# Performance work log

Hardware: AMD Instinct MI355X
Metric: run time of the kernel (lower is better)

The kernel has to match this reference:

```python
import jax, jax.numpy as jnp
import numpy as np

NEURON_CDECAY = 0.5
NEURON_VDECAY = 0.75
NEURON_VTH = 0.5
SPIKE_PSEUDO_GRAD_WINDOW = 0.5

@jax.custom_vjp
def pseudo_spike(v):
    return (v > NEURON_VTH).astype(v.dtype)

def _ps_fwd(v):
    return pseudo_spike(v), v

def _ps_bwd(v, g):
    return (g * (jnp.abs(v - NEURON_VTH) < SPIKE_PSEUDO_GRAD_WINDOW).astype(g.dtype),)

pseudo_spike.defvjp(_ps_fwd, _ps_bwd)

def conv1d(x, w, b):
    # x: (B, Cin, L), w: (Cout, Cin, K), stride 2, VALID padding
    y = jax.lax.conv_general_dilated(x, w, window_strides=(2,), padding='VALID',
                                     dimension_numbers=('NCH', 'OIH', 'NCH'))
    return y + b[None, :, None]

def neuron(syn_out, u, v, s):
    u = u * NEURON_CDECAY + syn_out
    v = v * NEURON_VDECAY * (1.0 - s) + u
    s = pseudo_spike(v)
    return u, v, s

def setup_inputs() -> dict:
    key = jax.random.key(0)
    ks = jax.random.split(key, 18)
    B, T, L = 4096, 50, 360
    h1, h2, h3, A = 256, 256, 128, 2
    def w(k, shape, fan_in):
        bound = 1.0 / np.sqrt(fan_in)
        return jax.random.uniform(k, shape, jnp.float32, -bound, bound)
    return {
        'normal_spikes': (jax.random.uniform(ks[0], (B, 6, T)) < 0.5).astype(jnp.float32),
        'scan_spikes': (jax.random.uniform(ks[1], (B, 1, L, T)) < 0.5).astype(jnp.float32),
        'batch_size': B,
        'conv1_w': w(ks[2], (5, 1, 5), 5),   'conv1_b': w(ks[3], (5,), 5),
        'conv2_w': w(ks[4], (5, 5, 5), 25),  'conv2_b': w(ks[5], (5,), 25),
        'conv3_w': w(ks[6], (5, 5, 5), 25),  'conv3_b': w(ks[7], (5,), 25),
        'fc1_w': w(ks[8], (h1, 216), 216),   'fc1_b': w(ks[9], (h1,), 216),
        'fc2_w': w(ks[10], (h2, h1), h1),    'fc2_b': w(ks[11], (h2,), h1),
        'fc3_w': w(ks[12], (h3, h2), h2),    'fc3_b': w(ks[13], (h3,), h2),
        'fc4_w': w(ks[14], (A, h3), h3),     'fc4_b': w(ks[15], (A,), h3),
    }

def reference(normal_spikes, scan_spikes, batch_size,
              conv1_w, conv1_b, conv2_w, conv2_b, conv3_w, conv3_b,
              fc1_w, fc1_b, fc2_w, fc2_b, fc3_w, fc3_b, fc4_w, fc4_b):
    B = batch_size
    T = normal_spikes.shape[-1]
    A = fc4_w.shape[0]
    # time-major sequences for lax.scan
    scan_seq = jnp.moveaxis(scan_spikes, -1, 0)    # (T, B, 1, 360)
    norm_seq = jnp.moveaxis(normal_spikes, -1, 0)  # (T, B, 6)

    z = lambda *s: jnp.zeros(s, jnp.float32)
    init = (
        (z(B, 5, 178), z(B, 5, 178), z(B, 5, 178)),
        (z(B, 5, 87),  z(B, 5, 87),  z(B, 5, 87)),
        (z(B, 5, 42),  z(B, 5, 42),  z(B, 5, 42)),
        (z(B, 256), z(B, 256), z(B, 256)),
        (z(B, 256), z(B, 256), z(B, 256)),
        (z(B, 128), z(B, 128), z(B, 128)),
        (z(B, A),   z(B, A),   z(B, A)),
        z(B, A),
    )

    def step(carry, xs):
        c1, c2, c3, f1, f2, f3, f4, acc = carry
        scan_x, norm_x = xs
        c1 = neuron(conv1d(scan_x, conv1_w, conv1_b), *c1)
        c2 = neuron(conv1d(c1[2], conv2_w, conv2_b), *c2)
        c3 = neuron(conv1d(c2[2], conv3_w, conv3_b), *c3)
        comb = jnp.concatenate([c3[2].reshape(B, -1), norm_x], axis=1)  # (B, 216)
        f1 = neuron(comb @ fc1_w.T + fc1_b, *f1)
        f2 = neuron(f1[2] @ fc2_w.T + fc2_b, *f2)
        f3 = neuron(f2[2] @ fc3_w.T + fc3_b, *f3)
        f4 = neuron(f3[2] @ fc4_w.T + fc4_b, *f4)
        acc = acc + f4[2]
        return (c1, c2, c3, f1, f2, f3, f4, acc), None

    carry, _ = jax.lax.scan(step, init, (scan_seq, norm_seq))
    return carry[-1] / T
```

## Files before the change

kernel.cpp:

```cpp
#include <hip/hip_runtime.h>
#include <cstdint>
#include <cstddef>


#define NB 4096
#define MTOT (NB * 50)

__device__ __forceinline__ void neuron_update(float syn, float& u, float& v, float& s) {
    u = u * 0.5f + syn;
    v = v * 0.75f * (1.0f - s) + u;
    s = (v > 0.5f) ? 1.0f : 0.0f;
}

__global__ __launch_bounds__(192) void conv1_kernel(
    const float* __restrict__ x, const float* __restrict__ w1,
    const float* __restrict__ b1, unsigned long long* __restrict__ S1)
{
    __shared__ float xl[9000];
    const int tid = threadIdx.x;
    const int b = blockIdx.x;
    const int j = tid;
    const int lbase = (j < 178) ? 2 * j : 354;

    float wr[25], br[5];
#pragma unroll
    for (int q = 0; q < 25; ++q) wr[q] = w1[q];
#pragma unroll
    for (int o = 0; o < 5; ++o) br[o] = b1[o];

    float u[5], v[5], s[5];
#pragma unroll
    for (int o = 0; o < 5; ++o) { u[o] = 0.f; v[o] = 0.f; s[o] = 0.f; }

    const float* xb = x + (size_t)b * 18000;
    for (int half = 0; half < 2; ++half) {
        const int t0 = half * 25;
        __syncthreads();
        for (int e = tid; e < 9000; e += 192)
            xl[e] = xb[(e / 25) * 50 + t0 + (e % 25)];
        __syncthreads();
        for (int dt = 0; dt < 25; ++dt) {
            const int t = t0 + dt;
            float xv[5];
#pragma unroll
            for (int k = 0; k < 5; ++k) xv[k] = xl[(lbase + k) * 25 + dt];
#pragma unroll
            for (int o = 0; o < 5; ++o) {
                float syn = 0.f;
#pragma unroll
                for (int k = 0; k < 5; ++k) syn += wr[o * 5 + k] * xv[k];
                syn += br[o];
                neuron_update(syn, u[o], v[o], s[o]);
                unsigned long long m = __ballot(j < 178 && s[o] > 0.5f);
                if ((tid & 63) == 0)
                    S1[(((size_t)b * 50 + t) * 5 + o) * 3 + (tid >> 6)] = m;
            }
        }
    }
}

__global__ __launch_bounds__(128) void conv2_kernel(
    const unsigned int* __restrict__ S1, const float* __restrict__ w2,
    const float* __restrict__ b2, unsigned int* __restrict__ S2)
{
    __shared__ unsigned int s1l[1501];
    const int tid = threadIdx.x;
    const int b = blockIdx.x;

    float wr[125], br[5];
#pragma unroll
    for (int q = 0; q < 125; ++q) wr[q] = w2[q];
#pragma unroll
    for (int o = 0; o < 5; ++o) br[o] = b2[o];

    const unsigned int* src = S1 + (size_t)b * 1500;
    for (int e = tid; e < 1500; e += 128) s1l[e] = src[e];
    __syncthreads();

    const int p = (tid < 87) ? 2 * tid : 172;
    const int pw = p >> 5, ps = p & 31;

    float u[5], v[5], s[5];
#pragma unroll
    for (int o = 0; o < 5; ++o) { u[o] = 0.f; v[o] = 0.f; s[o] = 0.f; }

    for (int t = 0; t < 50; ++t) {
        float xv[25];
#pragma unroll
        for (int ci = 0; ci < 5; ++ci) {
            const int base = (t * 5 + ci) * 6 + pw;
            unsigned long long bits =
                ((((unsigned long long)s1l[base + 1]) << 32) | (unsigned long long)s1l[base]) >> ps;
#pragma unroll
            for (int k = 0; k < 5; ++k)
                xv[ci * 5 + k] = ((bits >> k) & 1ULL) ? 1.0f : 0.0f;
        }
#pragma unroll
        for (int o = 0; o < 5; ++o) {
            float syn = 0.f;
#pragma unroll
            for (int q = 0; q < 25; ++q) syn += wr[o * 25 + q] * xv[q];
            syn += br[o];
            neuron_update(syn, u[o], v[o], s[o]);
            unsigned long long m = __ballot(tid < 87 && s[o] > 0.5f);
            const size_t outb = (((size_t)b * 50 + t) * 5 + o) * 3;
            if (tid == 0) {
                S2[outb]     = (unsigned int)m;
                S2[outb + 1] = (unsigned int)(m >> 32);
            }
            if (tid == 64) S2[outb + 2] = (unsigned int)m;
        }
    }
}

__global__ __launch_bounds__(64) void conv3_kernel(
    const unsigned int* __restrict__ S2, const float* __restrict__ w3,
    const float* __restrict__ b3, const float* __restrict__ normal,
    unsigned int* __restrict__ ST0)
{
    __shared__ unsigned int s2l[751];
    const int tid = threadIdx.x;
    const int b = blockIdx.x;

    float wr[125], br[5];
#pragma unroll
    for (int q = 0; q < 125; ++q) wr[q] = w3[q];
#pragma unroll
    for (int o = 0; o < 5; ++o) br[o] = b3[o];

    const unsigned int* src = S2 + (size_t)b * 750;
    for (int e = tid; e < 750; e += 64) s2l[e] = src[e];
    __syncthreads();

    const int p = (tid < 42) ? 2 * tid : 82;
    const int pw = p >> 5, ps = p & 31;

    float u[5], v[5], s[5];
#pragma unroll
    for (int o = 0; o < 5; ++o) { u[o] = 0.f; v[o] = 0.f; s[o] = 0.f; }

    for (int t = 0; t < 50; ++t) {
        float xv[25];
#pragma unroll
        for (int ci = 0; ci < 5; ++ci) {
            const int base = (t * 5 + ci) * 3 + pw;
            unsigned long long bits =
                ((((unsigned long long)s2l[base + 1]) << 32) | (unsigned long long)s2l[base]) >> ps;
#pragma unroll
            for (int k = 0; k < 5; ++k)
                xv[ci * 5 + k] = ((bits >> k) & 1ULL) ? 1.0f : 0.0f;
        }
        unsigned long long m[5];
#pragma unroll
        for (int o = 0; o < 5; ++o) {
            float syn = 0.f;
#pragma unroll
            for (int q = 0; q < 25; ++q) syn += wr[o * 25 + q] * xv[q];
            syn += br[o];
            neuron_update(syn, u[o], v[o], s[o]);
            m[o] = __ballot(tid < 42 && s[o] > 0.5f);
        }
        const unsigned long long nm =
            __ballot(tid < 6 && normal[((size_t)b * 6 + tid) * 50 + t] > 0.5f);
        if (tid == 0) {
            const unsigned long long r0 = m[0] | (m[1] << 42);
            const unsigned long long r1 = (m[1] >> 22) | (m[2] << 20) | (m[3] << 62);
            const unsigned long long r2 = (m[3] >> 2) | (m[4] << 40);
            const unsigned long long r3 = (m[4] >> 24) | (nm << 18);
            const size_t mrow = (size_t)b * 50 + t;
            ST0[0 * (size_t)MTOT + mrow] = (unsigned int)r0;
            ST0[1 * (size_t)MTOT + mrow] = (unsigned int)(r0 >> 32);
            ST0[2 * (size_t)MTOT + mrow] = (unsigned int)r1;
            ST0[3 * (size_t)MTOT + mrow] = (unsigned int)(r1 >> 32);
            ST0[4 * (size_t)MTOT + mrow] = (unsigned int)r2;
            ST0[5 * (size_t)MTOT + mrow] = (unsigned int)(r2 >> 32);
            ST0[6 * (size_t)MTOT + mrow] = (unsigned int)r3;
        }
    }
}

__global__ __launch_bounds__(256) void transpose_w_kernel(
    const float* __restrict__ W, float* __restrict__ Wt, int N, int KREAL, int KPAD)
{
    const int idx = blockIdx.x * 256 + threadIdx.x;
    if (idx >= KPAD * N) return;
    const int k = idx / N, n = idx % N;
    Wt[idx] = (k < KREAL) ? W[(size_t)n * KREAL + k] : 0.f;
}

__global__ __launch_bounds__(256) void sgemm_bits_kernel(
    const uint32_t* __restrict__ bitsT,
    const float* __restrict__ Wt,
    const float* __restrict__ bias,
    float* __restrict__ syn,
    int Ntot, int KT, int row0)
{
    const int tid = threadIdx.x;
    const int mloc = blockIdx.x * 256 + tid;
    const int mg = row0 + mloc;
    const int nbase = blockIdx.y * 32;

    uint32_t aw[8];
#pragma unroll
    for (int w = 0; w < 8; ++w)
        aw[w] = (w < KT) ? bitsT[(size_t)w * MTOT + mg] : 0u;

    float acc[32];
#pragma unroll
    for (int j = 0; j < 32; ++j) acc[j] = 0.f;

    const float* wt = Wt + nbase;
    for (int kt = 0; kt < KT; ++kt) {
        const uint32_t abit = aw[kt];
        const float* wk = wt + (size_t)(kt * 32) * Ntot;
#pragma unroll
        for (int kk = 0; kk < 32; ++kk) {
            const float a = (float)((abit >> kk) & 1u);
            const float* wr = wk + (size_t)kk * Ntot;
#pragma unroll
            for (int j = 0; j < 32; ++j)
                acc[j] = fmaf(a, wr[j], acc[j]);
        }
    }

    float* so = syn + (size_t)mloc * Ntot + nbase;
    const float* bs = bias + nbase;
#pragma unroll
    for (int q = 0; q < 8; ++q) {
        float4 ov;
        ov.x = acc[q * 4 + 0] + bs[q * 4 + 0];
        ov.y = acc[q * 4 + 1] + bs[q * 4 + 1];
        ov.z = acc[q * 4 + 2] + bs[q * 4 + 2];
        ov.w = acc[q * 4 + 3] + bs[q * 4 + 3];
        *reinterpret_cast<float4*>(so + q * 4) = ov;
    }
}

__global__ __launch_bounds__(256) void fc_scanT_kernel(
    const float* __restrict__ syn,
    uint32_t* __restrict__ SFT,
    int b0)
{
    const int tid = threadIdx.x;
    const int lane = tid & 63;
    const int ob = tid >> 6;
    const int bl = blockIdx.x;
    const int o = ob * 64 + lane;

    float u = 0.f, v = 0.f, s = 0.f;
    for (int t = 0; t < 50; ++t) {
        const float sv = syn[((size_t)bl * 50 + t) * 256 + o];
        neuron_update(sv, u, v, s);
        const unsigned long long m = __ballot(s > 0.5f);
        if (lane == 0) {
            const size_t row = (size_t)(b0 + bl) * 50 + t;
            SFT[(size_t)(2 * ob) * MTOT + row]     = (uint32_t)m;
            SFT[(size_t)(2 * ob + 1) * MTOT + row] = (uint32_t)(m >> 32);
        }
    }
}

__global__ __launch_bounds__(256) void fc_scan128_kernel(
    const float* __restrict__ syn,
    unsigned long long* __restrict__ SF,
    int b0)
{
    const int tid = threadIdx.x;
    const int wid = blockIdx.x * 4 + (tid >> 6);
    const int lane = tid & 63;
    const int bl = wid >> 1;
    const int ob = wid & 1;
    const int o = ob * 64 + lane;

    float u = 0.f, v = 0.f, s = 0.f;
    for (int t = 0; t < 50; ++t) {
        const float sv = syn[((size_t)bl * 50 + t) * 128 + o];
        neuron_update(sv, u, v, s);
        const unsigned long long m = __ballot(s > 0.5f);
        if (lane == 0) SF[((size_t)(b0 + bl) * 50 + t) * 2 + ob] = m;
    }
}

__global__ __launch_bounds__(256) void fc4_gemm_kernel(
    const unsigned long long* __restrict__ SF3, const float* __restrict__ W,
    const float* __restrict__ bias, float* __restrict__ syn4)
{
    const int m = blockIdx.x * 256 + threadIdx.x;
    const unsigned long long w0 = SF3[(size_t)m * 2];
    const unsigned long long w1 = SF3[(size_t)m * 2 + 1];
    float a0 = 0.f, a1 = 0.f;
#pragma unroll
    for (int i = 0; i < 64; ++i) {
        const float bit = ((w0 >> i) & 1ULL) ? 1.f : 0.f;
        a0 = fmaf(bit, W[i], a0);
        a1 = fmaf(bit, W[128 + i], a1);
    }
#pragma unroll
    for (int i = 0; i < 64; ++i) {
        const float bit = ((w1 >> i) & 1ULL) ? 1.f : 0.f;
        a0 = fmaf(bit, W[64 + i], a0);
        a1 = fmaf(bit, W[192 + i], a1);
    }
    syn4[(size_t)m * 2]     = a0 + bias[0];
    syn4[(size_t)m * 2 + 1] = a1 + bias[1];
}

__global__ __launch_bounds__(64) void fc4_scan_kernel(
    const float* __restrict__ syn4, float* __restrict__ out)
{
    const int b = blockIdx.x * 64 + threadIdx.x;
    float u0 = 0.f, v0 = 0.f, s0 = 0.f, acc0 = 0.f;
    float u1 = 0.f, v1 = 0.f, s1 = 0.f, acc1 = 0.f;
    for (int t = 0; t < 50; ++t) {
        const float x0 = syn4[((size_t)b * 50 + t) * 2];
        const float x1 = syn4[((size_t)b * 50 + t) * 2 + 1];
        neuron_update(x0, u0, v0, s0); acc0 += s0;
        neuron_update(x1, u1, v1, s1); acc1 += s1;
    }
    out[b * 2]     = acc0 / 50.0f;
    out[b * 2 + 1] = acc1 / 50.0f;
}

extern "C" void kernel_launch(void* const* d_in, const int* in_sizes, int n_in,
                              void* d_out, int out_size, void* d_ws, size_t ws_size,
                              hipStream_t stream) {
    (void)in_sizes; (void)n_in; (void)out_size;
    const float* normal = (const float*)d_in[0];
    const float* xscan  = (const float*)d_in[1];
    const float* w1  = (const float*)d_in[3];
    const float* b1  = (const float*)d_in[4];
    const float* w2  = (const float*)d_in[5];
    const float* b2  = (const float*)d_in[6];
    const float* w3  = (const float*)d_in[7];
    const float* b3  = (const float*)d_in[8];
    const float* fw1 = (const float*)d_in[9];
    const float* fb1 = (const float*)d_in[10];
    const float* fw2 = (const float*)d_in[11];
    const float* fb2 = (const float*)d_in[12];
    const float* fw3 = (const float*)d_in[13];
    const float* fb3 = (const float*)d_in[14];
    const float* fw4 = (const float*)d_in[15];
    const float* fb4 = (const float*)d_in[16];
    float* out = (float*)d_out;

    char* wp = (char*)d_ws;
    size_t off = 0;
    auto take = [&](size_t bytes) -> void* {
        void* p = wp + off;
        off += (bytes + 255) & ~(size_t)255;
        return p;
    };
    float* Wt1 = (float*)take((size_t)224 * 256 * 4);
    float* Wt2 = (float*)take((size_t)256 * 256 * 4);
    float* Wt3 = (float*)take((size_t)256 * 128 * 4);
    unsigned long long* S1  = (unsigned long long*)take((size_t)NB * 50 * 15 * 8);
    unsigned int*       S2  = (unsigned int*)take((size_t)NB * 50 * 15 * 4);
    uint32_t* ST0 = (uint32_t*)take((size_t)8 * MTOT * 4);
    uint32_t* ST1 = (uint32_t*)take((size_t)8 * MTOT * 4);
    uint32_t* ST2 = (uint32_t*)take((size_t)8 * MTOT * 4);
    unsigned long long* SF3 = (unsigned long long*)take((size_t)MTOT * 2 * 8);
    float*              syn4 = (float*)take((size_t)MTOT * 2 * 4);

    int chunk = NB;
    while (chunk > 128 && off + (size_t)chunk * 50 * 256 * 4 > ws_size) chunk >>= 1;
    float* syn = (float*)take((size_t)chunk * 50 * 256 * 4);

    transpose_w_kernel<<<(224 * 256 + 255) / 256, 256, 0, stream>>>(fw1, Wt1, 256, 216, 224);
    transpose_w_kernel<<<(256 * 256 + 255) / 256, 256, 0, stream>>>(fw2, Wt2, 256, 256, 256);
    transpose_w_kernel<<<(256 * 128 + 255) / 256, 256, 0, stream>>>(fw3, Wt3, 128, 256, 256);

    conv1_kernel<<<NB, 192, 0, stream>>>(xscan, w1, b1, S1);
    conv2_kernel<<<NB, 128, 0, stream>>>((const unsigned int*)S1, w2, b2, S2);
    conv3_kernel<<<NB, 64, 0, stream>>>(S2, w3, b3, normal, ST0);

    for (int b0 = 0; b0 < NB; b0 += chunk) {
        sgemm_bits_kernel<<<dim3(chunk * 50 / 256, 8), 256, 0, stream>>>(
            ST0, Wt1, fb1, syn, 256, 7, b0 * 50);
        fc_scanT_kernel<<<chunk, 256, 0, stream>>>(syn, ST1, b0);
    }
    for (int b0 = 0; b0 < NB; b0 += chunk) {
        sgemm_bits_kernel<<<dim3(chunk * 50 / 256, 8), 256, 0, stream>>>(
            ST1, Wt2, fb2, syn, 256, 8, b0 * 50);
        fc_scanT_kernel<<<chunk, 256, 0, stream>>>(syn, ST2, b0);
    }
    for (int b0 = 0; b0 < NB; b0 += chunk) {
        sgemm_bits_kernel<<<dim3(chunk * 50 / 256, 4), 256, 0, stream>>>(
            ST2, Wt3, fb3, syn, 128, 8, b0 * 50);
        fc_scan128_kernel<<<chunk / 2, 256, 0, stream>>>(syn, SF3, b0);
    }
    fc4_gemm_kernel<<<MTOT / 256, 256, 0, stream>>>(SF3, fw4, fb4, syn4);
    fc4_scan_kernel<<<NB / 64, 64, 0, stream>>>(syn4, out);
}
```

Before: 1.609 ms.

## Replace bit-packed FC activations with dense float rows and register-tiled SGEMM

Spikes feeding fc1 and fc2 are now stored as dense float rows (row-major, K padded) instead of transposed bit-planes. A new templated SGEMM has each thread own one output column and 32 rows, holding 32 weights in registers and reading A rows as wavefront-uniform broadcasts. The conv stages now run inside the batch-chunk loop with the FC stages, and workspace is sized per chunk. This trades the bit-unpack FMA loop for much more activation memory traffic (float instead of bits) in exchange for broadcast loads and better register reuse.

```diff
diff --git a/kernel.cpp b/kernel.cpp
--- a/kernel.cpp
+++ b/kernel.cpp
@@ -116,7 +116,7 @@
 __global__ __launch_bounds__(64) void conv3_kernel(
     const unsigned int* __restrict__ S2, const float* __restrict__ w3,
     const float* __restrict__ b3, const float* __restrict__ normal,
-    unsigned int* __restrict__ ST0)
+    float* __restrict__ A0)
 {
     __shared__ unsigned int s2l[751];
     const int tid = threadIdx.x;
@@ -150,7 +150,7 @@
             for (int k = 0; k < 5; ++k)
                 xv[ci * 5 + k] = ((bits >> k) & 1ULL) ? 1.0f : 0.0f;
         }
-        unsigned long long m[5];
+        float* arow = A0 + ((size_t)b * 50 + t) * 224;
 #pragma unroll
         for (int o = 0; o < 5; ++o) {
             float syn = 0.f;
@@ -158,24 +158,10 @@
             for (int q = 0; q < 25; ++q) syn += wr[o * 25 + q] * xv[q];
             syn += br[o];
             neuron_update(syn, u[o], v[o], s[o]);
-            m[o] = __ballot(tid < 42 && s[o] > 0.5f);
-        }
-        const unsigned long long nm =
-            __ballot(tid < 6 && normal[((size_t)b * 6 + tid) * 50 + t] > 0.5f);
-        if (tid == 0) {
-            const unsigned long long r0 = m[0] | (m[1] << 42);
-            const unsigned long long r1 = (m[1] >> 22) | (m[2] << 20) | (m[3] << 62);
-            const unsigned long long r2 = (m[3] >> 2) | (m[4] << 40);
-            const unsigned long long r3 = (m[4] >> 24) | (nm << 18);
-            const size_t mrow = (size_t)b * 50 + t;
-            ST0[0 * (size_t)MTOT + mrow] = (unsigned int)r0;
-            ST0[1 * (size_t)MTOT + mrow] = (unsigned int)(r0 >> 32);
-            ST0[2 * (size_t)MTOT + mrow] = (unsigned int)r1;
-            ST0[3 * (size_t)MTOT + mrow] = (unsigned int)(r1 >> 32);
-            ST0[4 * (size_t)MTOT + mrow] = (unsigned int)r2;
-            ST0[5 * (size_t)MTOT + mrow] = (unsigned int)(r2 >> 32);
-            ST0[6 * (size_t)MTOT + mrow] = (unsigned int)r3;
-        }
+            if (tid < 42) arow[o * 42 + tid] = s[o];
+        }
+        if (tid < 6)  arow[210 + tid] = normal[((size_t)b * 6 + tid) * 50 + t];
+        if (tid < 8)  arow[216 + tid] = 0.f;
     }
 }
 
@@ -188,75 +174,58 @@
     Wt[idx] = (k < KREAL) ? W[(size_t)n * KREAL + k] : 0.f;
 }
 
-__global__ __launch_bounds__(256) void sgemm_bits_kernel(
-    const uint32_t* __restrict__ bitsT,
+template <int NTOT, int KPAD>
+__global__ __launch_bounds__(256, 4) void sgemm_f_kernel(
+    const float* __restrict__ A,
     const float* __restrict__ Wt,
     const float* __restrict__ bias,
-    float* __restrict__ syn,
-    int Ntot, int KT, int row0)
-{
-    const int tid = threadIdx.x;
-    const int mloc = blockIdx.x * 256 + tid;
-    const int mg = row0 + mloc;
-    const int nbase = blockIdx.y * 32;
-
-    uint32_t aw[8];
-#pragma unroll
-    for (int w = 0; w < 8; ++w)
-        aw[w] = (w < KT) ? bitsT[(size_t)w * MTOT + mg] : 0u;
+    float* __restrict__ syn)
+{
+    constexpr int KT = KPAD / 32;
+    constexpr int GROUPS = 256 / NTOT;
+    const int tid = threadIdx.x;
+    const int n = tid & (NTOT - 1);
+    const int grp = tid / NTOT;
+    const int mbase = __builtin_amdgcn_readfirstlane(
+        blockIdx.x * (32 * GROUPS) + grp * 32);
+
+    const float* aBase = A + (size_t)mbase * KPAD;
 
     float acc[32];
 #pragma unroll
-    for (int j = 0; j < 32; ++j) acc[j] = 0.f;
-
-    const float* wt = Wt + nbase;
+    for (int i = 0; i < 32; ++i) acc[i] = 0.f;
+
     for (int kt = 0; kt < KT; ++kt) {
-        const uint32_t abit = aw[kt];
-        const float* wk = wt + (size_t)(kt * 32) * Ntot;
-#pragma unroll
-        for (int kk = 0; kk < 32; ++kk) {
-            const float a = (float)((abit >> kk) & 1u);
-            const float* wr = wk + (size_t)kk * Ntot;
-#pragma unroll
-            for (int j = 0; j < 32; ++j)
-                acc[j] = fmaf(a, wr[j], acc[j]);
-        }
-    }
-
-    float* so = syn + (size_t)mloc * Ntot + nbase;
-    const float* bs = bias + nbase;
-#pragma unroll
-    for (int q = 0; q < 8; ++q) {
-        float4 ov;
-        ov.x = acc[q * 4 + 0] + bs[q * 4 + 0];
-        ov.y = acc[q * 4 + 1] + bs[q * 4 + 1];
-        ov.z = acc[q * 4 + 2] + bs[q * 4 + 2];
-        ov.w = acc[q * 4 + 3] + bs[q * 4 + 3];
-        *reinterpret_cast<float4*>(so + q * 4) = ov;
-    }
-}
-
-__global__ __launch_bounds__(256) void fc_scanT_kernel(
+        float w[32];
+#pragma unroll
+        for (int kk = 0; kk < 32; ++kk)
+            w[kk] = Wt[(size_t)(kt * 32 + kk) * NTOT + n];
+#pragma unroll
+        for (int mi = 0; mi < 32; ++mi) {
+            const float* ar = aBase + mi * KPAD + kt * 32;
+#pragma unroll
+            for (int kk = 0; kk < 32; ++kk)
+                acc[mi] = fmaf(ar[kk], w[kk], acc[mi]);
+        }
+    }
+
+    const float bs = bias[n];
+#pragma unroll
+    for (int mi = 0; mi < 32; ++mi)
+        syn[(size_t)(mbase + mi) * NTOT + n] = acc[mi] + bs;
+}
+
+__global__ __launch_bounds__(256) void fc_scanF_kernel(
     const float* __restrict__ syn,
-    uint32_t* __restrict__ SFT,
-    int b0)
-{
-    const int tid = threadIdx.x;
-    const int lane = tid & 63;
-    const int ob = tid >> 6;
+    float* __restrict__ Aout)
+{
+    const int o = threadIdx.x;
     const int bl = blockIdx.x;
-    const int o = ob * 64 + lane;
-
     float u = 0.f, v = 0.f, s = 0.f;
     for (int t = 0; t < 50; ++t) {
-        const float sv = syn[((size_t)bl * 50 + t) * 256 + o];
-        neuron_update(sv, u, v, s);
-        const unsigned long long m = __ballot(s > 0.5f);
-        if (lane == 0) {
-            const size_t row = (size_t)(b0 + bl) * 50 + t;
-            SFT[(size_t)(2 * ob) * MTOT + row]     = (uint32_t)m;
-            SFT[(size_t)(2 * ob + 1) * MTOT + row] = (uint32_t)(m >> 32);
-        }
+        const size_t r = (size_t)bl * 50 + t;
+        neuron_update(syn[r * 256 + o], u, v, s);
+        Aout[r * 256 + o] = s;
     }
 }
 
@@ -353,41 +322,41 @@
     float* Wt1 = (float*)take((size_t)224 * 256 * 4);
     float* Wt2 = (float*)take((size_t)256 * 256 * 4);
     float* Wt3 = (float*)take((size_t)256 * 128 * 4);
-    unsigned long long* S1  = (unsigned long long*)take((size_t)NB * 50 * 15 * 8);
-    unsigned int*       S2  = (unsigned int*)take((size_t)NB * 50 * 15 * 4);
-    uint32_t* ST0 = (uint32_t*)take((size_t)8 * MTOT * 4);
-    uint32_t* ST1 = (uint32_t*)take((size_t)8 * MTOT * 4);
-    uint32_t* ST2 = (uint32_t*)take((size_t)8 * MTOT * 4);
     unsigned long long* SF3 = (unsigned long long*)take((size_t)MTOT * 2 * 8);
-    float*              syn4 = (float*)take((size_t)MTOT * 2 * 4);
-
+    float* syn4 = (float*)take((size_t)MTOT * 2 * 4);
+
+    const size_t PER_B = 50 * (15 * 8 + 15 * 4 + 224 * 4 + 256 * 4 + 256 * 4) + 5 * 256;
     int chunk = NB;
-    while (chunk > 128 && off + (size_t)chunk * 50 * 256 * 4 > ws_size) chunk >>= 1;
-    float* syn = (float*)take((size_t)chunk * 50 * 256 * 4);
+    while (chunk > 128 && off + (size_t)chunk * PER_B > ws_size) chunk >>= 1;
+
+    unsigned long long* S1  = (unsigned long long*)take((size_t)chunk * 50 * 15 * 8);
+    unsigned int*       S2  = (unsigned int*)take((size_t)chunk * 50 * 15 * 4);
+    float* A0   = (float*)take((size_t)chunk * 50 * 224 * 4);
+    float* Abuf = (float*)take((size_t)chunk * 50 * 256 * 4);
+    float* syn  = (float*)take((size_t)chunk * 50 * 256 * 4);
 
     transpose_w_kernel<<<(224 * 256 + 255) / 256, 256, 0, stream>>>(fw1, Wt1, 256, 216, 224);
     transpose_w_kernel<<<(256 * 256 + 255) / 256, 256, 0, stream>>>(fw2, Wt2, 256, 256, 256);
     transpose_w_kernel<<<(256 * 128 + 255) / 256, 256, 0, stream>>>(fw3, Wt3, 128, 256, 256);
 
-    conv1_kernel<<<NB, 192, 0, stream>>>(xscan, w1, b1, S1);
-    conv2_kernel<<<NB, 128, 0, stream>>>((const unsigned int*)S1, w2, b2, S2);
-    conv3_kernel<<<NB, 64, 0, stream>>>(S2, w3, b3, normal, ST0);
-
     for (int b0 = 0; b0 < NB; b0 += chunk) {
-        sgemm_bits_kernel<<<dim3(chunk * 50 / 256, 8), 256, 0, stream>>>(
-            ST0, Wt1, fb1, syn, 256, 7, b0 * 50);
-        fc_scanT_kernel<<<chunk, 256, 0, stream>>>(syn, ST1, b0);
-    }
-    for (int b0 = 0; b0 < NB; b0 += chunk) {
-        sgemm_bits_kernel<<<dim3(chunk * 50 / 256, 8), 256, 0, stream>>>(
-            ST1, Wt2, fb2, syn, 256, 8, b0 * 50);
-        fc_scanT_kernel<<<chunk, 256, 0, stream>>>(syn, ST2, b0);
-    }
-    for (int b0 = 0; b0 < NB; b0 += chunk) {
-        sgemm_bits_kernel<<<dim3(chunk * 50 / 256, 4), 256, 0, stream>>>(
-            ST2, Wt3, fb3, syn, 128, 8, b0 * 50);
+        conv1_kernel<<<chunk, 192, 0, stream>>>(
+            xscan + (size_t)b0 * 18000, w1, b1, S1);
+        conv2_kernel<<<chunk, 128, 0, stream>>>(
+            (const unsigned int*)S1, w2, b2, S2);
+        conv3_kernel<<<chunk, 64, 0, stream>>>(
+            S2, w3, b3, normal + (size_t)b0 * 300, A0);
+
+        sgemm_f_kernel<256, 224><<<chunk * 50 / 32, 256, 0, stream>>>(A0, Wt1, fb1, syn);
+        fc_scanF_kernel<<<chunk, 256, 0, stream>>>(syn, Abuf);
+
+        sgemm_f_kernel<256, 256><<<chunk * 50 / 32, 256, 0, stream>>>(Abuf, Wt2, fb2, syn);
+        fc_scanF_kernel<<<chunk, 256, 0, stream>>>(syn, Abuf);
+
+        sgemm_f_kernel<128, 256><<<chunk * 50 / 64, 256, 0, stream>>>(Abuf, Wt3, fb3, syn);
         fc_scan128_kernel<<<chunk / 2, 256, 0, stream>>>(syn, SF3, b0);
     }
+
     fc4_gemm_kernel<<<MTOT / 256, 256, 0, stream>>>(SF3, fw4, fb4, syn4);
     fc4_scan_kernel<<<NB / 64, 64, 0, stream>>>(syn4, out);
 }
```

Result: slower. 4.505 ms (+179.9%).

## Replace bit-sgemm with LDS-tiled register-blocked packed-FMA GEMM

Applied to the files above, without the earlier changes.

The per-thread bit-driven SGEMM, which re-read weight rows from global memory for every output row, is replaced by a templated kernel. It stages 32x128 weight tiles into double-buffered LDS via global_load_lds and computes a 16x8 register tile per thread with v_pk_fma_f32. The A bit-rows are prefetched one k-tile ahead and the three per-layer chunk loops are merged into one loop. This cuts global weight traffic and doubles FMA throughput per instruction, at the cost of higher register pressure and reliance on inline asm.

```diff
diff --git a/kernel.cpp b/kernel.cpp
--- a/kernel.cpp
+++ b/kernel.cpp
@@ -5,6 +5,8 @@
 
 #define NB 4096
 #define MTOT (NB * 50)
+
+typedef __attribute__((ext_vector_type(2))) float f32x2;
 
 __device__ __forceinline__ void neuron_update(float syn, float& u, float& v, float& s) {
     u = u * 0.5f + syn;
@@ -188,58 +190,105 @@
     Wt[idx] = (k < KREAL) ? W[(size_t)n * KREAL + k] : 0.f;
 }
 
-__global__ __launch_bounds__(256) void sgemm_bits_kernel(
+template <int NTOT, int KT>
+__global__ __launch_bounds__(256, 2) void pk_gemm_kernel(
     const uint32_t* __restrict__ bitsT,
     const float* __restrict__ Wt,
     const float* __restrict__ bias,
     float* __restrict__ syn,
-    int Ntot, int KT, int row0)
-{
-    const int tid = threadIdx.x;
-    const int mloc = blockIdx.x * 256 + tid;
-    const int mg = row0 + mloc;
-    const int nbase = blockIdx.y * 32;
-
-    uint32_t aw[8];
-#pragma unroll
-    for (int w = 0; w < 8; ++w)
-        aw[w] = (w < KT) ? bitsT[(size_t)w * MTOT + mg] : 0u;
-
-    float acc[32];
-#pragma unroll
-    for (int j = 0; j < 32; ++j) acc[j] = 0.f;
-
-    const float* wt = Wt + nbase;
+    int row0)
+{
+    __shared__ __align__(16) float blds[2][32 * 128];
+
+    const int tid = threadIdx.x;
+    const int lane = tid & 63;
+    const int wid = tid >> 6;
+    const int tm = tid & 15;
+    const int tn = tid >> 4;
+    const int m0 = blockIdx.x * 256;
+    const int nbase = blockIdx.y * 128;
+
+    auto stage = [&](int kt, int buf) {
+#pragma unroll
+        for (int j = 0; j < 4; ++j) {
+            const int c = (j * 4 + wid) * 64 + lane;
+            const int row = c >> 5, col = c & 31;
+            const float* src = Wt + (size_t)(kt * 32 + row) * NTOT + nbase + col * 4;
+            float* dst = &blds[buf][0] + (size_t)(j * 4 + wid) * 256 + lane * 4;
+            __builtin_amdgcn_global_load_lds(
+                (const __attribute__((address_space(1))) uint32_t*)src,
+                (__attribute__((address_space(3))) uint32_t*)dst, 16, 0, 0);
+        }
+    };
+
+    const int rowA = row0 + m0 + tm * 16;
+    auto loadA = [&](int kt, uint4& q0, uint4& q1, uint4& q2, uint4& q3) {
+        const uint32_t* p = bitsT + (size_t)kt * MTOT + rowA;
+        q0 = *reinterpret_cast<const uint4*>(p);
+        q1 = *reinterpret_cast<const uint4*>(p + 4);
+        q2 = *reinterpret_cast<const uint4*>(p + 8);
+        q3 = *reinterpret_cast<const uint4*>(p + 12);
+    };
+
+    uint4 A0, A1, A2, A3, N0, N1, N2, N3;
+    loadA(0, A0, A1, A2, A3);
+    stage(0, 0);
+
+    f32x2 acc[16][4];
+#pragma unroll
+    for (int mi = 0; mi < 16; ++mi)
+#pragma unroll
+        for (int r2 = 0; r2 < 4; ++r2) acc[mi][r2] = (f32x2){0.f, 0.f};
+
     for (int kt = 0; kt < KT; ++kt) {
-        const uint32_t abit = aw[kt];
-        const float* wk = wt + (size_t)(kt * 32) * Ntot;
+        __syncthreads();
+        if (kt + 1 < KT) {
+            stage(kt + 1, (kt + 1) & 1);
+            loadA(kt + 1, N0, N1, N2, N3);
+        }
+
+        uint awv[16] = {A0.x, A0.y, A0.z, A0.w, A1.x, A1.y, A1.z, A1.w,
+                        A2.x, A2.y, A2.z, A2.w, A3.x, A3.y, A3.z, A3.w};
+        const float* bt = &blds[kt & 1][0];
+
 #pragma unroll
         for (int kk = 0; kk < 32; ++kk) {
-            const float a = (float)((abit >> kk) & 1u);
-            const float* wr = wk + (size_t)kk * Ntot;
-#pragma unroll
-            for (int j = 0; j < 32; ++j)
-                acc[j] = fmaf(a, wr[j], acc[j]);
-        }
-    }
-
-    float* so = syn + (size_t)mloc * Ntot + nbase;
-    const float* bs = bias + nbase;
-#pragma unroll
-    for (int q = 0; q < 8; ++q) {
-        float4 ov;
-        ov.x = acc[q * 4 + 0] + bs[q * 4 + 0];
-        ov.y = acc[q * 4 + 1] + bs[q * 4 + 1];
-        ov.z = acc[q * 4 + 2] + bs[q * 4 + 2];
-        ov.w = acc[q * 4 + 3] + bs[q * 4 + 3];
-        *reinterpret_cast<float4*>(so + q * 4) = ov;
+            f32x2 w2[4];
+#pragma unroll
+            for (int r2 = 0; r2 < 4; ++r2)
+                w2[r2] = *reinterpret_cast<const f32x2*>(bt + kk * 128 + tn * 8 + r2 * 2);
+            f32x2 av = {0.f, 0.f};
+#pragma unroll
+            for (int mi = 0; mi < 16; ++mi) {
+                av.x = (float)((awv[mi] >> kk) & 1u);
+#pragma unroll
+                for (int r2 = 0; r2 < 4; ++r2)
+                    asm("v_pk_fma_f32 %0, %1, %2, %0 op_sel_hi:[0,1,1]"
+                        : "+v"(acc[mi][r2]) : "v"(av), "v"(w2[r2]));
+            }
+        }
+        if (kt + 1 < KT) { A0 = N0; A1 = N1; A2 = N2; A3 = N3; }
+    }
+
+    const int nb = nbase + tn * 8;
+    float bsv[8];
+#pragma unroll
+    for (int q = 0; q < 8; ++q) bsv[q] = bias[nb + q];
+#pragma unroll
+    for (int mi = 0; mi < 16; ++mi) {
+        float* so = syn + (size_t)(m0 + tm * 16 + mi) * NTOT + nb;
+        float4 o0, o1;
+        o0.x = acc[mi][0].x + bsv[0]; o0.y = acc[mi][0].y + bsv[1];
+        o0.z = acc[mi][1].x + bsv[2]; o0.w = acc[mi][1].y + bsv[3];
+        o1.x = acc[mi][2].x + bsv[4]; o1.y = acc[mi][2].y + bsv[5];
+        o1.z = acc[mi][3].x + bsv[6]; o1.w = acc[mi][3].y + bsv[7];
+        *reinterpret_cast<float4*>(so) = o0;
+        *reinterpret_cast<float4*>(so + 4) = o1;
     }
 }
 
 __global__ __launch_bounds__(256) void fc_scanT_kernel(
-    const float* __restrict__ syn,
-    uint32_t* __restrict__ SFT,
-    int b0)
+    const float* __restrict__ syn, uint32_t* __restrict__ SFT, int b0)
 {
     const int tid = threadIdx.x;
     const int lane = tid & 63;
@@ -261,9 +310,7 @@
 }
 
 __global__ __launch_bounds__(256) void fc_scan128_kernel(
-    const float* __restrict__ syn,
-    unsigned long long* __restrict__ SF,
-    int b0)
+    const float* __restrict__ syn, unsigned long long* __restrict__ SF, int b0)
 {
     const int tid = threadIdx.x;
     const int wid = blockIdx.x * 4 + (tid >> 6);
@@ -374,20 +421,19 @@
     conv3_kernel<<<NB, 64, 0, stream>>>(S2, w3, b3, normal, ST0);
 
     for (int b0 = 0; b0 < NB; b0 += chunk) {
-        sgemm_bits_kernel<<<dim3(chunk * 50 / 256, 8), 256, 0, stream>>>(
-            ST0, Wt1, fb1, syn, 256, 7, b0 * 50);
+        pk_gemm_kernel<256, 7><<<dim3(chunk * 50 / 256, 2), 256, 0, stream>>>(
+            ST0, Wt1, fb1, syn, b0 * 50);
         fc_scanT_kernel<<<chunk, 256, 0, stream>>>(syn, ST1, b0);
-    }
-    for (int b0 = 0; b0 < NB; b0 += chunk) {
-        sgemm_bits_kernel<<<dim3(chunk * 50 / 256, 8), 256, 0, stream>>>(
-            ST1, Wt2, fb2, syn, 256, 8, b0 * 50);
+
+        pk_gemm_kernel<256, 8><<<dim3(chunk * 50 / 256, 2), 256, 0, stream>>>(
+            ST1, Wt2, fb2, syn, b0 * 50);
         fc_scanT_kernel<<<chunk, 256, 0, stream>>>(syn, ST2, b0);
-    }
-    for (int b0 = 0; b0 < NB; b0 += chunk) {
-        sgemm_bits_kernel<<<dim3(chunk * 50 / 256, 4), 256, 0, stream>>>(
-            ST2, Wt3, fb3, syn, 128, 8, b0 * 50);
+
+        pk_gemm_kernel<128, 8><<<dim3(chunk * 50 / 256, 1), 256, 0, stream>>>(
+            ST2, Wt3, fb3, syn, b0 * 50);
         fc_scan128_kernel<<<chunk / 2, 256, 0, stream>>>(syn, SF3, b0);
     }
+
     fc4_gemm_kernel<<<MTOT / 256, 256, 0, stream>>>(SF3, fw4, fb4, syn4);
     fc4_scan_kernel<<<NB / 64, 64, 0, stream>>>(syn4, out);
 }
```

Result: no change. 1.601 ms (-0.5%).

## Replace scalar bit-GEMMs with split-bf16 MFMA GEMMs plus near-threshold repair

Applied to the files above, without the earlier changes.

The three FC layers' scalar FMA bit-GEMMs become MFMA kernels. Each fp32 weight is split into three bf16 parts, and the binary spike activations are expanded directly into bf16 fragments, with async global-to-LDS staging and a triple-buffered pipeline. The scan kernels flag neurons whose membrane potential came within a small delta of threshold, and a repair kernel recomputes those neurons exactly in fp32 and fixes their spike bits. The goal is to move the dominant GEMM cost onto matrix cores, at the cost of extra repair passes, atomics and more kernel launches. There is a risk if the split-bf16 error ever exceeds the delta.

```diff
diff --git a/kernel.cpp b/kernel.cpp
--- a/kernel.cpp
+++ b/kernel.cpp
@@ -5,6 +5,11 @@
 
 #define NB 4096
 #define MTOT (NB * 50)
+#define DELTA 1e-3f
+
+typedef __attribute__((ext_vector_type(8))) short bf16x8;
+typedef __attribute__((ext_vector_type(4))) float f32x4;
+typedef __attribute__((ext_vector_type(4))) uint32_t u32x4;
 
 __device__ __forceinline__ void neuron_update(float syn, float& u, float& v, float& s) {
     u = u * 0.5f + syn;
@@ -175,82 +180,168 @@
             ST0[4 * (size_t)MTOT + mrow] = (unsigned int)r2;
             ST0[5 * (size_t)MTOT + mrow] = (unsigned int)(r2 >> 32);
             ST0[6 * (size_t)MTOT + mrow] = (unsigned int)r3;
-        }
-    }
-}
-
-__global__ __launch_bounds__(256) void transpose_w_kernel(
-    const float* __restrict__ W, float* __restrict__ Wt, int N, int KREAL, int KPAD)
+            ST0[7 * (size_t)MTOT + mrow] = 0u;
+        }
+    }
+}
+
+__global__ __launch_bounds__(256) void pack_w_kernel(
+    const float* __restrict__ W, unsigned short* __restrict__ dst, int KREAL)
 {
     const int idx = blockIdx.x * 256 + threadIdx.x;
-    if (idx >= KPAD * N) return;
-    const int k = idx / N, n = idx % N;
-    Wt[idx] = (k < KREAL) ? W[(size_t)n * KREAL + k] : 0.f;
-}
-
-__global__ __launch_bounds__(256) void sgemm_bits_kernel(
+    const int n = idx >> 8, k = idx & 255;
+    const float w = (k < KREAL) ? W[(size_t)n * KREAL + k] : 0.f;
+    const uint32_t u0 = __float_as_uint(w);
+    const unsigned short h0 = (unsigned short)(u0 >> 16);
+    const float p0 = __uint_as_float(u0 & 0xFFFF0000u);
+    const float r1 = w - p0;
+    const uint32_t u1 = __float_as_uint(r1);
+    const unsigned short h1 = (unsigned short)(u1 >> 16);
+    const float p1 = __uint_as_float(u1 & 0xFFFF0000u);
+    const float r2 = r1 - p1;
+    const unsigned short h2 = (unsigned short)(__float_as_uint(r2) >> 16);
+
+    const int nb = n >> 7, row = n & 127;
+    const int kc = k >> 6, kl = k & 63;
+    const int kbyte = (kl * 2) ^ ((row & 7) << 4);
+    const size_t base = ((size_t)nb * 12 + (size_t)kc * 3) * 8192 + row * 64 + (kbyte >> 1);
+    dst[base] = h0;
+    dst[base + 8192] = h1;
+    dst[base + 16384] = h2;
+}
+
+__global__ __launch_bounds__(256, 3) void mfma_fc_kernel(
     const uint32_t* __restrict__ bitsT,
-    const float* __restrict__ Wt,
+    const unsigned short* __restrict__ wg,
     const float* __restrict__ bias,
     float* __restrict__ syn,
-    int Ntot, int KT, int row0)
-{
+    int Ntot, int row0)
+{
+    __shared__ __align__(16) unsigned short blds[3][8192];
+    __shared__ __align__(16) uint32_t bits_lds[1024];
+
     const int tid = threadIdx.x;
-    const int mloc = blockIdx.x * 256 + tid;
-    const int mg = row0 + mloc;
-    const int nbase = blockIdx.y * 32;
-
-    uint32_t aw[8];
-#pragma unroll
-    for (int w = 0; w < 8; ++w)
-        aw[w] = (w < KT) ? bitsT[(size_t)w * MTOT + mg] : 0u;
-
-    float acc[32];
-#pragma unroll
-    for (int j = 0; j < 32; ++j) acc[j] = 0.f;
-
-    const float* wt = Wt + nbase;
-    for (int kt = 0; kt < KT; ++kt) {
-        const uint32_t abit = aw[kt];
-        const float* wk = wt + (size_t)(kt * 32) * Ntot;
-#pragma unroll
-        for (int kk = 0; kk < 32; ++kk) {
-            const float a = (float)((abit >> kk) & 1u);
-            const float* wr = wk + (size_t)kk * Ntot;
-#pragma unroll
-            for (int j = 0; j < 32; ++j)
-                acc[j] = fmaf(a, wr[j], acc[j]);
-        }
-    }
-
-    float* so = syn + (size_t)mloc * Ntot + nbase;
-    const float* bs = bias + nbase;
-#pragma unroll
-    for (int q = 0; q < 8; ++q) {
-        float4 ov;
-        ov.x = acc[q * 4 + 0] + bs[q * 4 + 0];
-        ov.y = acc[q * 4 + 1] + bs[q * 4 + 1];
-        ov.z = acc[q * 4 + 2] + bs[q * 4 + 2];
-        ov.w = acc[q * 4 + 3] + bs[q * 4 + 3];
-        *reinterpret_cast<float4*>(so + q * 4) = ov;
-    }
-}
-
-__global__ __launch_bounds__(256) void fc_scanT_kernel(
+    const int lane = tid & 63;
+    const int wid = tid >> 6;
+    const int wm = wid >> 1, wn = wid & 1;
+    const int m0 = blockIdx.x * 128;
+    const int nb = blockIdx.y;
+    const int nbase = nb * 128;
+
+    {
+        const uint32_t* g = bitsT + (size_t)(tid >> 5) * MTOT + (row0 + m0) + (tid & 31) * 4;
+        uint32_t* l = bits_lds + wid * 256;
+        __builtin_amdgcn_global_load_lds(
+            (const __attribute__((address_space(1))) uint32_t*)g,
+            (__attribute__((address_space(3))) uint32_t*)l, 16, 0, 0);
+    }
+
+    auto stage = [&](int t_idx, int buf) {
+        const unsigned short* wt = wg + ((size_t)(nb * 12 + t_idx)) * 8192;
+#pragma unroll
+        for (int j = 0; j < 4; ++j) {
+            const char* g = (const char*)wt + j * 4096 + wid * 1024 + lane * 16;
+            char* l = (char*)&blds[buf][0] + j * 4096 + wid * 1024;
+            __builtin_amdgcn_global_load_lds(
+                (const __attribute__((address_space(1))) uint32_t*)g,
+                (__attribute__((address_space(3))) uint32_t*)l, 16, 0, 0);
+        }
+    };
+
+    stage(0, 0);
+    stage(1, 1);
+
+    f32x4 acc[4][4];
+#pragma unroll
+    for (int i = 0; i < 4; ++i)
+#pragma unroll
+        for (int j = 0; j < 4; ++j) acc[i][j] = (f32x4){0.f, 0.f, 0.f, 0.f};
+
+    union frag { u32x4 u; bf16x8 h; };
+    frag afr[4][2];
+
+#pragma unroll
+    for (int s = 0; s < 12; ++s) {
+        if (s < 11) asm volatile("s_waitcnt vmcnt(4)\ns_barrier" ::: "memory");
+        else        asm volatile("s_waitcnt vmcnt(0)\ns_barrier" ::: "memory");
+        if (s + 2 < 12) stage(s + 2, (s + 2) % 3);
+
+        const int kc = s / 3;
+        if ((s % 3) == 0) {
+#pragma unroll
+            for (int mi = 0; mi < 4; ++mi) {
+                const int row = wm * 64 + mi * 16 + (lane & 15);
+#pragma unroll
+                for (int kk = 0; kk < 2; ++kk) {
+                    const uint32_t wbits = bits_lds[(kc * 2 + kk) * 128 + row];
+                    const uint32_t bb = (wbits >> ((lane >> 4) * 8)) & 0xFFu;
+                    u32x4 e;
+#pragma unroll
+                    for (int j = 0; j < 4; ++j) {
+                        uint32_t r = ((bb >> (2 * j)) & 1u) ? 0x3F80u : 0u;
+                        if ((bb >> (2 * j + 1)) & 1u) r |= 0x3F800000u;
+                        e[j] = r;
+                    }
+                    afr[mi][kk].u = e;
+                }
+            }
+        }
+
+        const char* bt = (const char*)&blds[s % 3][0];
+        __builtin_amdgcn_s_setprio(1);
+#pragma unroll
+        for (int kk = 0; kk < 2; ++kk) {
+#pragma unroll
+            for (int ni = 0; ni < 4; ++ni) {
+                const int r = wn * 64 + ni * 16 + (lane & 15);
+                const int kb = kk * 64 + (lane >> 4) * 16;
+                const int off = r * 128 + (kb ^ ((r & 7) << 4));
+                bf16x8 bfr = *reinterpret_cast<const bf16x8*>(bt + off);
+#pragma unroll
+                for (int mi = 0; mi < 4; ++mi)
+                    acc[mi][ni] = __builtin_amdgcn_mfma_f32_16x16x32_bf16(
+                        afr[mi][kk].h, bfr, acc[mi][ni], 0, 0, 0);
+            }
+        }
+        __builtin_amdgcn_s_setprio(0);
+    }
+
+#pragma unroll
+    for (int ni = 0; ni < 4; ++ni) {
+        const int n = nbase + wn * 64 + ni * 16 + (lane & 15);
+        const float bs = bias[n];
+#pragma unroll
+        for (int mi = 0; mi < 4; ++mi) {
+            const int mr = m0 + wm * 64 + mi * 16 + ((lane >> 4) << 2);
+            float* dst = syn + (size_t)mr * Ntot + n;
+            f32x4 a = acc[mi][ni];
+#pragma unroll
+            for (int rr = 0; rr < 4; ++rr) dst[(size_t)rr * Ntot] = a[rr] + bs;
+        }
+    }
+}
+
+template <int N>
+__global__ __launch_bounds__(N) void fc_scan_flag_kernel(
     const float* __restrict__ syn,
     uint32_t* __restrict__ SFT,
-    int b0)
+    int b0,
+    uint32_t* __restrict__ list, unsigned int* __restrict__ cnt)
 {
     const int tid = threadIdx.x;
     const int lane = tid & 63;
     const int ob = tid >> 6;
     const int bl = blockIdx.x;
-    const int o = ob * 64 + lane;
+    const int o = tid;
 
     float u = 0.f, v = 0.f, s = 0.f;
+    bool flag = false;
     for (int t = 0; t < 50; ++t) {
-        const float sv = syn[((size_t)bl * 50 + t) * 256 + o];
-        neuron_update(sv, u, v, s);
+        const float sv = syn[((size_t)bl * 50 + t) * N + o];
+        u = u * 0.5f + sv;
+        v = v * 0.75f * (1.0f - s) + u;
+        flag |= (fabsf(v - 0.5f) < DELTA);
+        s = (v > 0.5f) ? 1.0f : 0.0f;
         const unsigned long long m = __ballot(s > 0.5f);
         if (lane == 0) {
             const size_t row = (size_t)(b0 + bl) * 50 + t;
@@ -258,36 +349,85 @@
             SFT[(size_t)(2 * ob + 1) * MTOT + row] = (uint32_t)(m >> 32);
         }
     }
-}
-
-__global__ __launch_bounds__(256) void fc_scan128_kernel(
-    const float* __restrict__ syn,
-    unsigned long long* __restrict__ SF,
-    int b0)
-{
-    const int tid = threadIdx.x;
-    const int wid = blockIdx.x * 4 + (tid >> 6);
-    const int lane = tid & 63;
-    const int bl = wid >> 1;
-    const int ob = wid & 1;
-    const int o = ob * 64 + lane;
-
-    float u = 0.f, v = 0.f, s = 0.f;
-    for (int t = 0; t < 50; ++t) {
-        const float sv = syn[((size_t)bl * 50 + t) * 128 + o];
-        neuron_update(sv, u, v, s);
-        const unsigned long long m = __ballot(s > 0.5f);
-        if (lane == 0) SF[((size_t)(b0 + bl) * 50 + t) * 2 + ob] = m;
+    const unsigned long long fm = __ballot(flag);
+    unsigned int base = 0;
+    if (lane == 0 && fm) base = atomicAdd(cnt, (unsigned int)__popcll(fm));
+    base = __shfl(base, 0);
+    if (flag) {
+        const unsigned int off = (unsigned int)__popcll(fm & ((1ULL << lane) - 1ULL));
+        list[base + off] = ((unsigned int)(b0 + bl) << 8) | (unsigned int)o;
+    }
+}
+
+template <int KT, int KREAL>
+__global__ __launch_bounds__(256) void repair_kernel(
+    const uint32_t* __restrict__ planesIn,
+    const float* __restrict__ W,
+    const float* __restrict__ bias,
+    uint32_t* __restrict__ planesOut,
+    const uint32_t* __restrict__ list,
+    const unsigned int* __restrict__ cnt)
+{
+    const int lane = threadIdx.x & 63;
+    const int wid = blockIdx.x * 4 + (threadIdx.x >> 6);
+    const int nwaves = gridDim.x * 4;
+    const unsigned int n = *cnt;
+
+    for (unsigned int idx = wid; idx < n; idx += nwaves) {
+        const uint32_t e = list[idx];
+        const int b = __builtin_amdgcn_readfirstlane((int)(e >> 8));
+        const int o = __builtin_amdgcn_readfirstlane((int)(e & 255u));
+        const int tl = (lane < 50) ? lane : 49;
+        const size_t row = (size_t)b * 50 + tl;
+
+        uint32_t wb[KT];
+#pragma unroll
+        for (int w = 0; w < KT; ++w) wb[w] = planesIn[(size_t)w * MTOT + row];
+
+        const float* wr = W + (size_t)o * KREAL;
+        float acc = 0.f;
+#pragma unroll
+        for (int kt = 0; kt < KT; ++kt) {
+#pragma unroll
+            for (int kk = 0; kk < 32; ++kk) {
+                const int k = kt * 32 + kk;
+                if (k < KREAL)
+                    acc = fmaf((float)((wb[kt] >> kk) & 1u), wr[k], acc);
+            }
+        }
+        const float syn_t = acc + bias[o];
+
+        float u = 0.f, v = 0.f, s = 0.f, mys = 0.f;
+#pragma unroll 1
+        for (int t = 0; t < 50; ++t) {
+            const float sv = __shfl(syn_t, t);
+            u = u * 0.5f + sv;
+            v = v * 0.75f * (1.0f - s) + u;
+            s = (v > 0.5f) ? 1.0f : 0.0f;
+            if (lane == t) mys = s;
+        }
+
+        if (lane < 50) {
+            uint32_t* wp = planesOut + (size_t)(o >> 5) * MTOT + row;
+            const uint32_t bit = 1u << (o & 31);
+            const bool prov = (*wp & bit) != 0u;
+            const bool ex = (mys > 0.5f);
+            if (prov != ex) atomicXor(wp, bit);
+        }
     }
 }
 
 __global__ __launch_bounds__(256) void fc4_gemm_kernel(
-    const unsigned long long* __restrict__ SF3, const float* __restrict__ W,
-    const float* __restrict__ bias, float* __restrict__ syn4)
+    const uint32_t* __restrict__ P3,
+    const float* __restrict__ W, const float* __restrict__ bias,
+    float* __restrict__ syn4)
 {
     const int m = blockIdx.x * 256 + threadIdx.x;
-    const unsigned long long w0 = SF3[(size_t)m * 2];
-    const unsigned long long w1 = SF3[(size_t)m * 2 + 1];
+    const unsigned long long w0 =
+        (unsigned long long)P3[m] | ((unsigned long long)P3[(size_t)MTOT + m] << 32);
+    const unsigned long long w1 =
+        (unsigned long long)P3[2 * (size_t)MTOT + m] |
+        ((unsigned long long)P3[3 * (size_t)MTOT + m] << 32);
     float a0 = 0.f, a1 = 0.f;
 #pragma unroll
     for (int i = 0; i < 64; ++i) {
@@ -350,44 +490,52 @@
         off += (bytes + 255) & ~(size_t)255;
         return p;
     };
-    float* Wt1 = (float*)take((size_t)224 * 256 * 4);
-    float* Wt2 = (float*)take((size_t)256 * 256 * 4);
-    float* Wt3 = (float*)take((size_t)256 * 128 * 4);
+    unsigned short* Wg1 = (unsigned short*)take((size_t)2 * 12 * 8192 * 2);
+    unsigned short* Wg2 = (unsigned short*)take((size_t)2 * 12 * 8192 * 2);
+    unsigned short* Wg3 = (unsigned short*)take((size_t)1 * 12 * 8192 * 2);
     unsigned long long* S1  = (unsigned long long*)take((size_t)NB * 50 * 15 * 8);
     unsigned int*       S2  = (unsigned int*)take((size_t)NB * 50 * 15 * 4);
     uint32_t* ST0 = (uint32_t*)take((size_t)8 * MTOT * 4);
     uint32_t* ST1 = (uint32_t*)take((size_t)8 * MTOT * 4);
     uint32_t* ST2 = (uint32_t*)take((size_t)8 * MTOT * 4);
-    unsigned long long* SF3 = (unsigned long long*)take((size_t)MTOT * 2 * 8);
-    float*              syn4 = (float*)take((size_t)MTOT * 2 * 4);
+    uint32_t* ST3 = (uint32_t*)take((size_t)4 * MTOT * 4);
+    float*    syn4 = (float*)take((size_t)MTOT * 2 * 4);
+    unsigned int* cnts = (unsigned int*)take(256);
+    uint32_t* list0 = (uint32_t*)take((size_t)NB * 256 * 4);
+    uint32_t* list1 = (uint32_t*)take((size_t)NB * 256 * 4);
+    uint32_t* list2 = (uint32_t*)take((size_t)NB * 128 * 4);
 
     int chunk = NB;
     while (chunk > 128 && off + (size_t)chunk * 50 * 256 * 4 > ws_size) chunk >>= 1;
     float* syn = (float*)take((size_t)chunk * 50 * 256 * 4);
 
-    transpose_w_kernel<<<(224 * 256 + 255) / 256, 256, 0, stream>>>(fw1, Wt1, 256, 216, 224);
-    transpose_w_kernel<<<(256 * 256 + 255) / 256, 256, 0, stream>>>(fw2, Wt2, 256, 256, 256);
-    transpose_w_kernel<<<(256 * 128 + 255) / 256, 256, 0, stream>>>(fw3, Wt3, 128, 256, 256);
+    hipMemsetAsync(cnts, 0, 12, stream);
+
+    pack_w_kernel<<<256, 256, 0, stream>>>(fw1, Wg1, 216);
+    pack_w_kernel<<<256, 256, 0, stream>>>(fw2, Wg2, 256);
+    pack_w_kernel<<<128, 256, 0, stream>>>(fw3, Wg3, 256);
 
     conv1_kernel<<<NB, 192, 0, stream>>>(xscan, w1, b1, S1);
     conv2_kernel<<<NB, 128, 0, stream>>>((const unsigned int*)S1, w2, b2, S2);
     conv3_kernel<<<NB, 64, 0, stream>>>(S2, w3, b3, normal, ST0);
 
     for (int b0 = 0; b0 < NB; b0 += chunk) {
-        sgemm_bits_kernel<<<dim3(chunk * 50 / 256, 8), 256, 0, stream>>>(
-            ST0, Wt1, fb1, syn, 256, 7, b0 * 50);
-        fc_scanT_kernel<<<chunk, 256, 0, stream>>>(syn, ST1, b0);
-    }
-    for (int b0 = 0; b0 < NB; b0 += chunk) {
-        sgemm_bits_kernel<<<dim3(chunk * 50 / 256, 8), 256, 0, stream>>>(
-            ST1, Wt2, fb2, syn, 256, 8, b0 * 50);
-        fc_scanT_kernel<<<chunk, 256, 0, stream>>>(syn, ST2, b0);
-    }
-    for (int b0 = 0; b0 < NB; b0 += chunk) {
-        sgemm_bits_kernel<<<dim3(chunk * 50 / 256, 4), 256, 0, stream>>>(
-            ST2, Wt3, fb3, syn, 128, 8, b0 * 50);
-        fc_scan128_kernel<<<chunk / 2, 256, 0, stream>>>(syn, SF3, b0);
-    }
-    fc4_gemm_kernel<<<MTOT / 256, 256, 0, stream>>>(SF3, fw4, fb4, syn4);
+        mfma_fc_kernel<<<dim3(chunk * 50 / 128, 2), 256, 0, stream>>>(
+            ST0, Wg1, fb1, syn, 256, b0 * 50);
+        fc_scan_flag_kernel<256><<<chunk, 256, 0, stream>>>(syn, ST1, b0, list0, cnts + 0);
+        repair_kernel<7, 216><<<512, 256, 0, stream>>>(ST0, fw1, fb1, ST1, list0, cnts + 0);
+
+        mfma_fc_kernel<<<dim3(chunk * 50 / 128, 2), 256, 0, stream>>>(
+            ST1, Wg2, fb2, syn, 256, b0 * 50);
+        fc_scan_flag_kernel<256><<<chunk, 256, 0, stream>>>(syn, ST2, b0, list1, cnts + 1);
+        repair_kernel<8, 256><<<512, 256, 0, stream>>>(ST1, fw2, fb2, ST2, list1, cnts + 1);
+
+        mfma_fc_kernel<<<dim3(chunk * 50 / 128, 1), 256, 0, stream>>>(
+            ST2, Wg3, fb3, syn, 128, b0 * 50);
+        fc_scan_flag_kernel<128><<<chunk, 128, 0, stream>>>(syn, ST3, b0, list2, cnts + 2);
+        repair_kernel<8, 256><<<512, 256, 0, stream>>>(ST2, fw3, fb3, ST3, list2, cnts + 2);
+    }
+
+    fc4_gemm_kernel<<<MTOT / 256, 256, 0, stream>>>(ST3, fw4, fb4, syn4);
     fc4_scan_kernel<<<NB / 64, 64, 0, stream>>>(syn4, out);
 }
```

After: 1.782 ms. 1.11x slower.
